# Optimization experiments

Hardware: AMD Instinct MI355X
Metric: run time of the kernel (lower is better)

The kernel has to match this reference:

```python
import jax, jax.numpy as jnp
import numpy as np

# Dimensions (match init_kwargs / input_specs)
B, Hr, Wr, C, NH = 16, 64, 64, 512, 16
WS = 8                 # window size (square)
N = WS * WS            # tokens per window
TAB = 2 * WS - 1       # bias table size
DH = C // NH           # head dim


def layernorm(x, g, b, eps=1e-5):
    mu = jnp.mean(x, axis=-1, keepdims=True)
    var = jnp.var(x, axis=-1, keepdims=True)
    return (x - mu) * jax.lax.rsqrt(var + eps) * g + b


def setup_inputs() -> dict:
    key = jax.random.key(0)
    ks = jax.random.split(key, 10)
    p = lambda k, shape: jax.random.normal(k, shape, jnp.float32) * 0.02
    # relative coordinates within a window: (2, N, N), values in [-(WS-1), WS-1]
    coords = np.stack(np.meshgrid(np.arange(WS), np.arange(WS), indexing='ij'))
    cf = coords.reshape(2, -1)
    rel = cf[:, :, None] - cf[:, None, :]
    radius_idx = (rel[0] % TAB).astype(np.int32)   # torch negative-wrap indexing
    azimuth_idx = (rel[1] % TAB).astype(np.int32)
    return dict(
        x=jax.random.normal(ks[0], (B, Hr * Wr, C), jnp.float32),
        theta_max=jnp.asarray(np.pi / 2, jnp.float32),
        norm1_g=jnp.ones((C,), jnp.float32), norm1_b=jnp.zeros((C,), jnp.float32),
        qkv_w=p(ks[1], (3 * C, C)), qkv_b=jnp.zeros((3 * C,), jnp.float32),
        a_p=p(ks[2], (TAB, NH)), b_p=p(ks[3], (TAB, NH)),
        a_r=p(ks[4], (TAB, NH)), b_r=p(ks[5], (TAB, NH)),
        proj_w=p(ks[6], (C, C)), proj_b=jnp.zeros((C,), jnp.float32),
        norm2_g=jnp.ones((C,), jnp.float32), norm2_b=jnp.zeros((C,), jnp.float32),
        fc1_w=p(ks[7], (4 * C, C)), fc1_b=jnp.zeros((4 * C,), jnp.float32),
        fc2_w=p(ks[8], (C, 4 * C)), fc2_b=jnp.zeros((C,), jnp.float32),
        radius_idx=jnp.asarray(radius_idx), azimuth_idx=jnp.asarray(azimuth_idx),
    )


def reference(x, theta_max, norm1_g, norm1_b, qkv_w, qkv_b, a_p, b_p, a_r, b_r,
              proj_w, proj_b, norm2_g, norm2_b, fc1_w, fc1_b, fc2_w, fc2_b,
              radius_idx, azimuth_idx):
    scale = DH ** -0.5
    shortcut = x
    h = layernorm(x, norm1_g, norm1_b).reshape(B, Hr, Wr, C)
    # window partition -> (B*nW, N, C)
    h = h.reshape(B, Hr // WS, WS, Wr // WS, WS, C)
    h = h.transpose(0, 1, 3, 2, 4, 5).reshape(-1, N, C)
    # qkv: (3, B_, NH, N, DH)
    qkv = (h @ qkv_w.T + qkv_b).reshape(-1, N, 3, NH, DH).transpose(2, 0, 3, 1, 4)
    q, k, v = qkv[0] * scale, qkv[1], qkv[2]
    attn = jnp.einsum('whqd,whkd->whqk', q, k)
    # trig relative position bias (phi over azimuth, theta over radius)
    rel_r = jnp.where(radius_idx < WS, radius_idx, radius_idx - TAB).astype(x.dtype)
    rel_a = jnp.where(azimuth_idx < WS, azimuth_idx, azimuth_idx - TAB).astype(x.dtype)
    ph_a = (rel_a * (2.0 * np.pi) / Wr)[..., None]      # (N, N, 1)
    ph_r = (rel_r * theta_max / Hr)[..., None]
    A_phi = a_p[azimuth_idx] * jnp.cos(ph_a) + b_p[azimuth_idx] * jnp.sin(ph_a)
    A_th = a_r[radius_idx] * jnp.cos(ph_r) + b_r[radius_idx] * jnp.sin(ph_r)
    attn = attn + jnp.transpose(A_phi + A_th, (2, 0, 1))[None]  # (1, NH, N, N)
    attn = jax.nn.softmax(attn, axis=-1)
    out = jnp.einsum('whqk,whkd->whqd', attn, v)
    out = out.transpose(0, 2, 1, 3).reshape(-1, N, C)
    out = out @ proj_w.T + proj_b
    # window reverse -> (B, Hr*Wr, C)
    out = out.reshape(B, Hr // WS, Wr // WS, WS, WS, C)
    out = out.transpose(0, 1, 3, 2, 4, 5).reshape(B, Hr * Wr, C)
    x = shortcut + out
    # MLP with residual
    h2 = layernorm(x, norm2_g, norm2_b)
    h2 = jax.nn.gelu(h2 @ fc1_w.T + fc1_b, approximate=False)
    h2 = h2 @ fc2_w.T + fc2_b
    return x + h2
```

## Files before the change

### kernel.cpp

```cpp
#include <hip/hip_runtime.h>

#define Bq    16
#define HRq   64
#define WRq   64
#define Cq    512
#define NHq   16
#define WSq   8
#define NTq   64
#define TABq  15
#define DHq   32
#define Mq    65536
#define QKVLD 1536

typedef __attribute__((ext_vector_type(8))) short   bfrag;
typedef __attribute__((ext_vector_type(4))) float   facc;
typedef __attribute__((ext_vector_type(4))) float   f4v;
typedef __attribute__((ext_vector_type(8))) unsigned short u16x8;

__device__ __forceinline__ unsigned short f2bf(float f) {
  union { float f; unsigned int i; } c; c.f = f;
  unsigned int i = c.i;
  return (unsigned short)((i + 0x7FFFu + ((i >> 16) & 1u)) >> 16);
}

#define GLD16(GP, LP) __builtin_amdgcn_global_load_lds(                         \
    (__attribute__((address_space(1))) void*)((void*)(GP)),                     \
    (__attribute__((address_space(3))) void*)((void*)(LP)), 16, 0, 0)

__global__ __launch_bounds__(256) void cast_bf16_kernel(
    const float* __restrict__ s, unsigned short* __restrict__ d, int n4) {
  int i = blockIdx.x * 256 + threadIdx.x;
  if (i < n4) {
    f4v v = ((const f4v*)s)[i];
    unsigned short o0 = f2bf(v[0]), o1 = f2bf(v[1]), o2 = f2bf(v[2]), o3 = f2bf(v[3]);
    unsigned long long packed = (unsigned long long)o0 | ((unsigned long long)o1 << 16) |
                                ((unsigned long long)o2 << 32) | ((unsigned long long)o3 << 48);
    ((unsigned long long*)d)[i] = packed;
  }
}

__global__ __launch_bounds__(256) void bias_kernel(
    const float* __restrict__ a_p, const float* __restrict__ b_p,
    const float* __restrict__ a_r, const float* __restrict__ b_r,
    const int* __restrict__ ridx, const int* __restrict__ aidx,
    const float* __restrict__ theta, float* __restrict__ bias) {
  int t = blockIdx.x * 256 + threadIdx.x;
  int h = t >> 12, ij = t & 4095;
  int ri = ridx[ij], ai = aidx[ij];
  float rel_r = (ri < WSq) ? (float)ri : (float)(ri - TABq);
  float rel_a = (ai < WSq) ? (float)ai : (float)(ai - TABq);
  float ph_a = rel_a * 6.283185307179586f / (float)WRq;
  float ph_r = rel_r * theta[0] / (float)HRq;
  float Aphi = a_p[ai * NHq + h] * cosf(ph_a) + b_p[ai * NHq + h] * sinf(ph_a);
  float Ath  = a_r[ri * NHq + h] * cosf(ph_r) + b_r[ri * NHq + h] * sinf(ph_r);
  bias[t] = Aphi + Ath;
}

template <int PERM>
__global__ __launch_bounds__(256) void ln_kernel(
    const float* __restrict__ x, const float* __restrict__ g, const float* __restrict__ b,
    unsigned short* __restrict__ out) {
  int row  = blockIdx.x * 4 + (threadIdx.x >> 6);
  int lane = threadIdx.x & 63;
  const float* xr = x + (size_t)row * Cq + lane * 8;
  f4v x0 = *(const f4v*)xr;
  f4v x1 = *(const f4v*)(xr + 4);
  float s = 0.f, q = 0.f;
#pragma unroll
  for (int e = 0; e < 4; ++e) { s += x0[e] + x1[e]; q += x0[e]*x0[e] + x1[e]*x1[e]; }
#pragma unroll
  for (int m = 1; m < 64; m <<= 1) { s += __shfl_xor(s, m, 64); q += __shfl_xor(q, m, 64); }
  float mu   = s * (1.0f / Cq);
  float var  = q * (1.0f / Cq) - mu * mu;
  float rstd = rsqrtf(var + 1e-5f);
  f4v g0 = *(const f4v*)(g + lane * 8);
  f4v g1 = *(const f4v*)(g + lane * 8 + 4);
  f4v b0 = *(const f4v*)(b + lane * 8);
  f4v b1 = *(const f4v*)(b + lane * 8 + 4);
  int orow = row;
  if (PERM) {
    int bb = row >> 12, y = (row >> 6) & 63, xx = row & 63;
    orow = ((bb * 8 + (y >> 3)) * 8 + (xx >> 3)) * 64 + ((y & 7) * 8 + (xx & 7));
  }
  u16x8 ov;
#pragma unroll
  for (int e = 0; e < 8; ++e) {
    float xe = (e < 4) ? x0[e] : x1[e - 4];
    float ge = (e < 4) ? g0[e] : g1[e - 4];
    float be = (e < 4) ? b0[e] : b1[e - 4];
    ov[e] = f2bf((xe - mu) * rstd * ge + be);
  }
  *(u16x8*)(out + (size_t)orow * Cq + lane * 8) = ov;
}

template <int MODE>
__global__ __launch_bounds__(256) void gemm_bt_kernel(
    const unsigned short* __restrict__ A, const unsigned short* __restrict__ W,
    const float* __restrict__ bias, void* __restrict__ outp,
    const float* __restrict__ resid, int K, int ldo) {
  __shared__ unsigned short As[128 * 64];
  __shared__ unsigned short Bs[128 * 64];
  const int t = threadIdx.x;
  const int w = t >> 6;
  const int wr = w >> 1, wc = w & 1;
  const int l15 = t & 15, l4 = (t & 63) >> 4;
  const int tn = blockIdx.x * 128;
  const int tm = blockIdx.y * 128;

  facc zero = {0.f, 0.f, 0.f, 0.f};
  facc acc[4][4];
#pragma unroll
  for (int i = 0; i < 4; ++i)
#pragma unroll
    for (int j = 0; j < 4; ++j) acc[i][j] = zero;

  for (int k0 = 0; k0 < K; k0 += 64) {
#pragma unroll
    for (int i = 0; i < 4; ++i) {
      int c = (i << 8) + t;
      int r = c >> 3, kc = (c & 7) << 3;
      GLD16(A + (size_t)(tm + r) * K + (k0 + kc), As + (size_t)((i << 8) + (w << 6)) * 8);
      GLD16(W + (size_t)(tn + r) * K + (k0 + kc), Bs + (size_t)((i << 8) + (w << 6)) * 8);
    }
    __syncthreads();
#pragma unroll
    for (int kk = 0; kk < 64; kk += 32) {
      bfrag af[4], bf[4];
#pragma unroll
      for (int mt = 0; mt < 4; ++mt)
        af[mt] = *(const bfrag*)(As + (wr * 64 + mt * 16 + l15) * 64 + kk + l4 * 8);
#pragma unroll
      for (int nt = 0; nt < 4; ++nt)
        bf[nt] = *(const bfrag*)(Bs + (wc * 64 + nt * 16 + l15) * 64 + kk + l4 * 8);
#pragma unroll
      for (int mt = 0; mt < 4; ++mt)
#pragma unroll
        for (int nt = 0; nt < 4; ++nt)
          acc[mt][nt] = __builtin_amdgcn_mfma_f32_16x16x32_bf16(af[mt], bf[nt], acc[mt][nt], 0, 0, 0);
    }
    __syncthreads();
  }

#pragma unroll
  for (int mt = 0; mt < 4; ++mt) {
#pragma unroll
    for (int nt = 0; nt < 4; ++nt) {
      int col = tn + wc * 64 + nt * 16 + l15;
      float bval = bias[col];
#pragma unroll
      for (int r = 0; r < 4; ++r) {
        int row = tm + wr * 64 + mt * 16 + l4 * 4 + r;
        float v = acc[mt][nt][r] + bval;
        if constexpr (MODE == 0) {
          ((unsigned short*)outp)[(size_t)row * ldo + col] = f2bf(v);
        } else if constexpr (MODE == 1) {
          int wm = row >> 6, tt = row & 63;
          int bb = wm >> 6, hw = (wm >> 3) & 7, ww = wm & 7;
          int orow = bb * 4096 + ((hw * 8 + (tt >> 3)) << 6) + ww * 8 + (tt & 7);
          float res = resid[(size_t)orow * ldo + col];
          ((float*)outp)[(size_t)orow * ldo + col] = v + res;
        } else if constexpr (MODE == 2) {
          float gl = 0.5f * v * (1.0f + erff(v * 0.7071067811865475f));
          ((unsigned short*)outp)[(size_t)row * ldo + col] = f2bf(gl);
        } else {
          float* o = (float*)outp + (size_t)row * ldo + col;
          *o += v;
        }
      }
    }
  }
}

__global__ __launch_bounds__(64) void attn_kernel(
    const unsigned short* __restrict__ qkv, const float* __restrict__ bias,
    unsigned short* __restrict__ outp) {
  __shared__ unsigned short P[64 * 64];
  __shared__ unsigned short V[64 * 32];
  const int lane = threadIdx.x;
  const int l15 = lane & 15, l4 = lane >> 4;
  const int win = blockIdx.x >> 4, h = blockIdx.x & 15;
  const unsigned short* qb = qkv + (size_t)(win * 64) * QKVLD + h * 32;
  const unsigned short* kb = qb + 512;
  const unsigned short* vb = qb + 1024;

#pragma unroll
  for (int i = 0; i < 4; ++i) {
    int c = i * 64 + lane;
    int r = c >> 2, kc = (c & 3) << 3;
    GLD16(vb + (size_t)r * QKVLD + kc, V + (size_t)i * 512);
  }

  bfrag qf[4], kf[4];
#pragma unroll
  for (int mt = 0; mt < 4; ++mt)
    qf[mt] = *(const bfrag*)(qb + (size_t)(mt * 16 + l15) * QKVLD + l4 * 8);
#pragma unroll
  for (int nt = 0; nt < 4; ++nt)
    kf[nt] = *(const bfrag*)(kb + (size_t)(nt * 16 + l15) * QKVLD + l4 * 8);
  facc zero = {0.f, 0.f, 0.f, 0.f};
  facc s[4][4];
#pragma unroll
  for (int mt = 0; mt < 4; ++mt)
#pragma unroll
    for (int nt = 0; nt < 4; ++nt) {
      s[mt][nt] = zero;
      s[mt][nt] = __builtin_amdgcn_mfma_f32_16x16x32_bf16(qf[mt], kf[nt], s[mt][nt], 0, 0, 0);
    }

  const float scale = 0.17677669529663687f;
  const float* bb = bias + h * 4096;
  float rinv[4][4];
#pragma unroll
  for (int mt = 0; mt < 4; ++mt) {
#pragma unroll
    for (int r = 0; r < 4; ++r) {
      int i = mt * 16 + l4 * 4 + r;
#pragma unroll
      for (int jt = 0; jt < 4; ++jt) {
        int j = jt * 16 + l15;
        s[mt][jt][r] = s[mt][jt][r] * scale + bb[i * 64 + j];
      }
      float rm = fmaxf(fmaxf(s[mt][0][r], s[mt][1][r]), fmaxf(s[mt][2][r], s[mt][3][r]));
      rm = fmaxf(rm, __shfl_xor(rm, 1, 64));
      rm = fmaxf(rm, __shfl_xor(rm, 2, 64));
      rm = fmaxf(rm, __shfl_xor(rm, 4, 64));
      rm = fmaxf(rm, __shfl_xor(rm, 8, 64));
      float sum = 0.f;
#pragma unroll
      for (int jt = 0; jt < 4; ++jt) {
        float e = __expf(s[mt][jt][r] - rm);
        s[mt][jt][r] = e;
        sum += e;
      }
      sum += __shfl_xor(sum, 1, 64);
      sum += __shfl_xor(sum, 2, 64);
      sum += __shfl_xor(sum, 4, 64);
      sum += __shfl_xor(sum, 8, 64);
      rinv[mt][r] = 1.0f / sum;
    }
  }

#pragma unroll
  for (int mt = 0; mt < 4; ++mt)
#pragma unroll
    for (int jt = 0; jt < 4; ++jt)
#pragma unroll
      for (int r = 0; r < 4; ++r) {
        int i = mt * 16 + l4 * 4 + r, j = jt * 16 + l15;
        int bofs = (i * 128 + j * 2) ^ ((i & 7) << 4);
        *(unsigned short*)((char*)P + bofs) = f2bf(s[mt][jt][r]);
      }
  __syncthreads();

  facc o[4][2];
#pragma unroll
  for (int mt = 0; mt < 4; ++mt)
#pragma unroll
    for (int nt = 0; nt < 2; ++nt) o[mt][nt] = zero;
#pragma unroll
  for (int kt = 0; kt < 2; ++kt) {
    bfrag pf[4];
#pragma unroll
    for (int mt = 0; mt < 4; ++mt) {
      int row = mt * 16 + l15;
      int bofs = (row * 128 + (kt * 32 + l4 * 8) * 2) ^ ((row & 7) << 4);
      pf[mt] = *(const bfrag*)((char*)P + bofs);
    }
    bfrag vf[2];
#pragma unroll
    for (int nt = 0; nt < 2; ++nt) {
      bfrag tv;
#pragma unroll
      for (int e = 0; e < 8; ++e) {
        int j = kt * 32 + l4 * 8 + e;
        tv[e] = (short)V[j * 32 + nt * 16 + l15];
      }
      vf[nt] = tv;
    }
#pragma unroll
    for (int mt = 0; mt < 4; ++mt)
#pragma unroll
      for (int nt = 0; nt < 2; ++nt)
        o[mt][nt] = __builtin_amdgcn_mfma_f32_16x16x32_bf16(pf[mt], vf[nt], o[mt][nt], 0, 0, 0);
  }

#pragma unroll
  for (int mt = 0; mt < 4; ++mt)
#pragma unroll
    for (int nt = 0; nt < 2; ++nt)
#pragma unroll
      for (int r = 0; r < 4; ++r) {
        int i = mt * 16 + l4 * 4 + r, d = nt * 16 + l15;
        float val = o[mt][nt][r] * rinv[mt][r];
        outp[(size_t)(win * 64 + i) * Cq + h * 32 + d] = f2bf(val);
      }
}

extern "C" void kernel_launch(void* const* d_in, const int* in_sizes, int n_in,
                              void* d_out, int out_size, void* d_ws, size_t ws_size,
                              hipStream_t stream) {
  const float* x     = (const float*)d_in[0];
  const float* theta = (const float*)d_in[1];
  const float* n1g   = (const float*)d_in[2];
  const float* n1b   = (const float*)d_in[3];
  const float* qkvw  = (const float*)d_in[4];
  const float* qkvb  = (const float*)d_in[5];
  const float* a_p   = (const float*)d_in[6];
  const float* b_p   = (const float*)d_in[7];
  const float* a_r   = (const float*)d_in[8];
  const float* b_r   = (const float*)d_in[9];
  const float* projw = (const float*)d_in[10];
  const float* projb = (const float*)d_in[11];
  const float* n2g   = (const float*)d_in[12];
  const float* n2b   = (const float*)d_in[13];
  const float* fc1w  = (const float*)d_in[14];
  const float* fc1b  = (const float*)d_in[15];
  const float* fc2w  = (const float*)d_in[16];
  const float* fc2b  = (const float*)d_in[17];
  const int* ridx    = (const int*)d_in[18];
  const int* aidx    = (const int*)d_in[19];
  float* out = (float*)d_out;

  char* ws = (char*)d_ws;
  unsigned short* lnbuf   = (unsigned short*)(ws);
  unsigned short* qkvbuf  = (unsigned short*)(ws + 67108864LL);
  unsigned short* attnbuf = (unsigned short*)(ws + 268435456LL);
  unsigned short* fc1buf  = (unsigned short*)(ws + 67108864LL);
  unsigned short* wq  = (unsigned short*)(ws + 335544320LL);
  unsigned short* wp  = (unsigned short*)(ws + 337117184LL);
  unsigned short* wf1 = (unsigned short*)(ws + 337641472LL);
  unsigned short* wf2 = (unsigned short*)(ws + 339738624LL);
  float* biasbuf = (float*)(ws + 341835776LL);

  cast_bf16_kernel<<<768, 256, 0, stream>>>(qkvw, wq, 786432 / 4);
  cast_bf16_kernel<<<256, 256, 0, stream>>>(projw, wp, 262144 / 4);
  cast_bf16_kernel<<<1024, 256, 0, stream>>>(fc1w, wf1, 1048576 / 4);
  cast_bf16_kernel<<<1024, 256, 0, stream>>>(fc2w, wf2, 1048576 / 4);
  bias_kernel<<<256, 256, 0, stream>>>(a_p, b_p, a_r, b_r, ridx, aidx, theta, biasbuf);

  ln_kernel<1><<<16384, 256, 0, stream>>>(x, n1g, n1b, lnbuf);
  gemm_bt_kernel<0><<<dim3(12, 512), 256, 0, stream>>>(lnbuf, wq, qkvb, qkvbuf, nullptr, 512, QKVLD);
  attn_kernel<<<16384, 64, 0, stream>>>(qkvbuf, biasbuf, attnbuf);
  gemm_bt_kernel<1><<<dim3(4, 512), 256, 0, stream>>>(attnbuf, wp, projb, out, x, 512, 512);
  ln_kernel<0><<<16384, 256, 0, stream>>>(out, n2g, n2b, lnbuf);
  gemm_bt_kernel<2><<<dim3(16, 512), 256, 0, stream>>>(lnbuf, wf1, fc1b, fc1buf, nullptr, 512, 2048);
  gemm_bt_kernel<3><<<dim3(4, 512), 256, 0, stream>>>(fc1buf, wf2, fc2b, out, nullptr, 2048, 512);
}
```

Baseline: 1.327 ms.

## Add XCD-aware block remap and wider-tile FC2 GEMM kernel

Adds a block-index remapping so that consecutive tiles land on the same XCD, aiming for better L2 reuse across all GEMMs. It also replaces the FC2 GEMM with a dedicated 512-thread kernel that uses 128x256 tiles. The wider tiles halve the number of A-tile reloads over the long K=2048 reduction. The larger tile uses more LDS (48KB) and halves the grid to 1024 blocks, which may lower occupancy.

```diff
diff --git a/kernel.cpp b/kernel.cpp
--- a/kernel.cpp
+++ b/kernel.cpp
@@ -26,6 +26,16 @@
 #define GLD16(GP, LP) __builtin_amdgcn_global_load_lds(                         \
     (__attribute__((address_space(1))) void*)((void*)(GP)),                     \
     (__attribute__((address_space(3))) void*)((void*)(LP)), 16, 0, 0)
+
+__device__ __forceinline__ void xcd_remap(int& bx, int& by) {
+  int gx = gridDim.x;
+  int nwg = gx * gridDim.y;
+  int d = by * gx + bx;
+  int cpx = nwg >> 3;
+  int l = (d & 7) * cpx + (d >> 3);
+  bx = l % gx;
+  by = l / gx;
+}
 
 __global__ __launch_bounds__(256) void cast_bf16_kernel(
     const float* __restrict__ s, unsigned short* __restrict__ d, int n4) {
@@ -104,8 +114,10 @@
   const int w = t >> 6;
   const int wr = w >> 1, wc = w & 1;
   const int l15 = t & 15, l4 = (t & 63) >> 4;
-  const int tn = blockIdx.x * 128;
-  const int tm = blockIdx.y * 128;
+  int bx = blockIdx.x, by = blockIdx.y;
+  xcd_remap(bx, by);
+  const int tn = bx * 128;
+  const int tm = by * 128;
 
   facc zero = {0.f, 0.f, 0.f, 0.f};
   facc acc[4][4];
@@ -162,10 +174,76 @@
         } else if constexpr (MODE == 2) {
           float gl = 0.5f * v * (1.0f + erff(v * 0.7071067811865475f));
           ((unsigned short*)outp)[(size_t)row * ldo + col] = f2bf(gl);
-        } else {
-          float* o = (float*)outp + (size_t)row * ldo + col;
-          *o += v;
         }
+      }
+    }
+  }
+}
+
+__global__ __launch_bounds__(512) void gemm_fc2_kernel(
+    const unsigned short* __restrict__ A, const unsigned short* __restrict__ W,
+    const float* __restrict__ bias, float* __restrict__ outp, int K, int ldo) {
+  __shared__ unsigned short As[128 * 64];
+  __shared__ unsigned short Bs[256 * 64];
+  const int t = threadIdx.x;
+  const int w = t >> 6;
+  const int wr = w >> 2, wc = w & 3;
+  const int l15 = t & 15, l4 = (t & 63) >> 4;
+  int bx = blockIdx.x, by = blockIdx.y;
+  xcd_remap(bx, by);
+  const int tn = bx * 256;
+  const int tm = by * 128;
+
+  facc zero = {0.f, 0.f, 0.f, 0.f};
+  facc acc[4][4];
+#pragma unroll
+  for (int i = 0; i < 4; ++i)
+#pragma unroll
+    for (int j = 0; j < 4; ++j) acc[i][j] = zero;
+
+  for (int k0 = 0; k0 < K; k0 += 64) {
+#pragma unroll
+    for (int i = 0; i < 2; ++i) {
+      int c = (i << 9) + t;
+      int r = c >> 3, kc = (c & 7) << 3;
+      GLD16(A + (size_t)(tm + r) * K + (k0 + kc), As + (size_t)((i << 9) + (w << 6)) * 8);
+    }
+#pragma unroll
+    for (int i = 0; i < 4; ++i) {
+      int c = (i << 9) + t;
+      int r = c >> 3, kc = (c & 7) << 3;
+      GLD16(W + (size_t)(tn + r) * K + (k0 + kc), Bs + (size_t)((i << 9) + (w << 6)) * 8);
+    }
+    __syncthreads();
+#pragma unroll
+    for (int kk = 0; kk < 64; kk += 32) {
+      bfrag af[4], bf[4];
+#pragma unroll
+      for (int mt = 0; mt < 4; ++mt)
+        af[mt] = *(const bfrag*)(As + (wr * 64 + mt * 16 + l15) * 64 + kk + l4 * 8);
+#pragma unroll
+      for (int nt = 0; nt < 4; ++nt)
+        bf[nt] = *(const bfrag*)(Bs + (wc * 64 + nt * 16 + l15) * 64 + kk + l4 * 8);
+#pragma unroll
+      for (int mt = 0; mt < 4; ++mt)
+#pragma unroll
+        for (int nt = 0; nt < 4; ++nt)
+          acc[mt][nt] = __builtin_amdgcn_mfma_f32_16x16x32_bf16(af[mt], bf[nt], acc[mt][nt], 0, 0, 0);
+    }
+    __syncthreads();
+  }
+
+#pragma unroll
+  for (int mt = 0; mt < 4; ++mt) {
+#pragma unroll
+    for (int nt = 0; nt < 4; ++nt) {
+      int col = tn + wc * 64 + nt * 16 + l15;
+      float bval = bias[col];
+#pragma unroll
+      for (int r = 0; r < 4; ++r) {
+        int row = tm + wr * 64 + mt * 16 + l4 * 4 + r;
+        float* o = outp + (size_t)row * ldo + col;
+        *o += acc[mt][nt][r] + bval;
       }
     }
   }
@@ -344,5 +422,5 @@
   gemm_bt_kernel<1><<<dim3(4, 512), 256, 0, stream>>>(attnbuf, wp, projb, out, x, 512, 512);
   ln_kernel<0><<<16384, 256, 0, stream>>>(out, n2g, n2b, lnbuf);
   gemm_bt_kernel<2><<<dim3(16, 512), 256, 0, stream>>>(lnbuf, wf1, fc1b, fc1buf, nullptr, 512, 2048);
-  gemm_bt_kernel<3><<<dim3(4, 512), 256, 0, stream>>>(fc1buf, wf2, fc2b, out, nullptr, 2048, 512);
-}
+  gemm_fc2_kernel<<<dim3(2, 512), 512, 0, stream>>>(fc1buf, wf2, fc2b, out, 2048, 512);
+}
```

Result: faster. 1.241 ms (-6.4%).
